# Performance work log

Measured on AMD Instinct MI355X. Metric: run time of the kernel, lower is better.

## Reference

```python
import jax, jax.numpy as jnp
import numpy as np

EPS = 1e-8
NEG = -1e7  # min_val used by masked_max


def _div_safe(a, b):
    return a / jnp.maximum(b, EPS)


def _masked_max(v, m, axis):
    mb = jnp.broadcast_to(m, v.shape)
    val = jnp.where(mb > 0, v, NEG).max(axis=axis)
    return val * mb.max(axis=axis)


def _masked_mean(v, m, axis):
    mb = jnp.broadcast_to(m, v.shape)
    return _div_safe((v * mb).sum(axis=axis), mb.sum(axis=axis))


def _cos_pairwise(v1, v2):
    # v1: (b,p,h), v2: (b,q,h) -> (b,p,q)
    n1 = jnp.linalg.norm(v1, axis=2, keepdims=True)
    n2 = jnp.linalg.norm(v2, axis=2, keepdims=True)
    dot = jnp.einsum('bph,bqh->bpq', v1, v2)
    return _div_safe(dot, n1 * n2.transpose(0, 2, 1))


def _mpm(v1, v2, w):
    # v1,v2: (b,L,h); w: (np,h) -> ((b,L,1), (b,L,np))
    dot = (v1 * v2).sum(-1)
    n = jnp.linalg.norm(v1, axis=-1) * jnp.linalg.norm(v2, axis=-1)
    mv1 = _div_safe(dot, n)[..., None]
    wv1 = w[None, None] * v1[:, :, None, :]  # (b,L,np,h)
    wv2 = w[None, None] * v2[:, :, None, :]
    dotm = (wv1 * wv2).sum(-1)
    nm = jnp.linalg.norm(wv1, axis=-1) * jnp.linalg.norm(wv2, axis=-1)
    return mv1, _div_safe(dotm, nm)


def _mpm_pairwise(v1, v2, w):
    # v1: (b,L1,h), v2: (b,L2,h), w: (np,h) -> (b,L1,L2,np)
    wv1 = w[None, :, None, :] * v1[:, None, :, :]  # (b,np,L1,h)
    wv2 = w[None, :, None, :] * v2[:, None, :, :]  # (b,np,L2,h)
    n1 = jnp.linalg.norm(wv1, axis=3, keepdims=True)
    n2 = jnp.linalg.norm(wv2, axis=3, keepdims=True)
    dot = jnp.einsum('bnph,bnqh->bnpq', wv1, wv2)
    res = _div_safe(dot, n1 * n2.transpose(0, 1, 3, 2))
    return res.transpose(0, 2, 3, 1)


def _bimpm(context_p, mask_p, context_h, mask_h, w_full, w_maxpool, w_att, w_max_att):
    b = context_p.shape[0]
    mask_p_h = mask_p[:, :, None] * mask_h[:, None, :]  # (b,Lp,Lh)
    mask_h_p = mask_p_h.transpose(0, 2, 1)
    context_p = context_p * mask_p[:, :, None]
    context_h = context_h * mask_h[:, :, None]

    cos = _cos_pairwise(context_p, context_h)  # (b,Lp,Lh)
    mv_p = [_masked_max(cos, mask_p_h, 2)[:, :, None],
            _masked_mean(cos, mask_p_h, 2)[:, :, None]]
    cos_t = cos.transpose(0, 2, 1)
    mv_h = [_masked_max(cos_t, mask_h_p, 2)[:, :, None],
            _masked_mean(cos_t, mask_h_p, 2)[:, :, None]]

    # full match (is_forward=True): match against last non-pad token
    idx_p = jnp.clip(mask_p.sum(1).astype(jnp.int32) - 1, 0)
    idx_h = jnp.clip(mask_h.sum(1).astype(jnp.int32) - 1, 0)
    last_p = context_p[jnp.arange(b), idx_p][:, None, :]  # (b,1,h)
    last_h = context_h[jnp.arange(b), idx_h][:, None, :]
    m1, mm = _mpm(context_p, jnp.broadcast_to(last_h, context_p.shape), w_full)
    mv_p += [m1, mm]
    m1, mm = _mpm(context_h, jnp.broadcast_to(last_p, context_h.shape), w_full)
    mv_h += [m1, mm]

    # maxpool match
    mv_max = _mpm_pairwise(context_p, context_h, w_maxpool)  # (b,Lp,Lh,np)
    mv_p += [_masked_max(mv_max, mask_p_h[..., None], 2),
             _masked_mean(mv_max, mask_p_h[..., None], 2)]
    mv_max_t = mv_max.transpose(0, 2, 1, 3)
    mv_h += [_masked_max(mv_max_t, mask_h_p[..., None], 2),
             _masked_mean(mv_max_t, mask_h_p[..., None], 2)]

    # attentive match
    att_h = context_h[:, None, :, :] * cos[..., None]  # (b,Lp,Lh,h)
    att_p = context_p[:, :, None, :] * cos[..., None]  # (b,Lp,Lh,h)
    att_mean_h = _div_safe(jnp.einsum('bpq,bqh->bph', cos, context_h),
                           cos.sum(2, keepdims=True))
    att_mean_p = _div_safe(jnp.einsum('bpq,bph->bqh', cos, context_p),
                           cos.sum(1, keepdims=True).transpose(0, 2, 1))
    m1, mm = _mpm(context_p, att_mean_h, w_att)
    mv_p += [m1, mm]
    m1, mm = _mpm(context_h, att_mean_p, w_att)
    mv_h += [m1, mm]

    # max attentive match
    att_max_h = _masked_max(att_h, mask_p_h[..., None], 2)  # (b,Lp,h)
    att_max_p = _masked_max(att_p.transpose(0, 2, 1, 3), mask_h_p[..., None], 2)  # (b,Lh,h)
    m1, mm = _mpm(context_p, att_max_h, w_max_att)
    mv_p += [m1, mm]
    m1, mm = _mpm(context_h, att_max_p, w_max_att)
    mv_h += [m1, mm]

    return jnp.concatenate(mv_p, axis=2), jnp.concatenate(mv_h, axis=2)


def setup_inputs() -> dict:
    B, LP, LH, H, NP = 32, 128, 128, 200, 20
    key = jax.random.key(0)
    ks = jax.random.split(key, 8)
    len_p = jax.random.randint(ks[0], (B,), LP // 2, LP + 1)
    len_h = jax.random.randint(ks[1], (B,), LH // 2, LH + 1)
    return {
        'context_p': jax.random.normal(ks[2], (B, LP, H), dtype=jnp.float32),
        'mask_p': (jnp.arange(LP)[None, :] < len_p[:, None]).astype(jnp.float32),
        'context_h': jax.random.normal(ks[3], (B, LH, H), dtype=jnp.float32),
        'mask_h': (jnp.arange(LH)[None, :] < len_h[:, None]).astype(jnp.float32),
        'w_full': jax.random.uniform(ks[4], (NP, H), dtype=jnp.float32),
        'w_maxpool': jax.random.uniform(ks[5], (NP, H), dtype=jnp.float32),
        'w_att': jax.random.uniform(ks[6], (NP, H), dtype=jnp.float32),
        'w_max_att': jax.random.uniform(ks[7], (NP, H), dtype=jnp.float32),
    }


def reference(context_p, mask_p, context_h, mask_h, w_full, w_maxpool, w_att, w_max_att):
    return _bimpm(context_p, mask_p, context_h, mask_h, w_full, w_maxpool, w_att, w_max_att)
```

## Files before the change

kernel.cpp:

```cpp
#include <hip/hip_runtime.h>
#include <hip/hip_bf16.h>


#define EPSF 1e-8f
#define NEGF -1e7f

constexpr int Bc = 32, Lc = 128, Hc = 200, NPc = 20, NCHc = 105;
constexpr int KP = 224;
constexpr size_t SLL = (size_t)Bc * Lc * Lc;

constexpr size_t OFF_COS    = 0;
constexpr size_t OFF_COST   = OFF_COS + SLL;
constexpr size_t OFF_NORMP  = OFF_COST + SLL;
constexpr size_t OFF_NORMH  = OFF_NORMP + (size_t)Bc * Lc;
constexpr size_t OFF_LENP   = OFF_NORMH + (size_t)Bc * Lc;
constexpr size_t OFF_LENH   = OFF_LENP + Bc;
constexpr size_t OFF_LASTP  = OFF_LENH + Bc;
constexpr size_t OFF_LASTH  = OFF_LASTP + (size_t)Bc * Hc;
constexpr size_t OFF_NWP    = OFF_LASTH + (size_t)Bc * Hc;
constexpr size_t OFF_NWH    = OFF_NWP + (size_t)Bc * NPc * Lc;
constexpr size_t OFF_MASKPF = OFF_NWH + (size_t)Bc * NPc * Lc;
constexpr size_t OFF_MASKHF = OFF_MASKPF + (size_t)Bc * Lc;
constexpr size_t OFF_FLAG   = OFF_MASKHF + (size_t)Bc * Lc;
constexpr size_t OFF_WT     = OFF_FLAG + 64;
constexpr size_t OFF_RPMAX  = OFF_WT + (size_t)Hc * 64;
constexpr size_t OFF_RPSUM  = OFF_RPMAX + 2 * (size_t)Bc * NPc * Lc;
constexpr size_t OFF_CPMAX  = OFF_RPSUM + 2 * (size_t)Bc * NPc * Lc;
constexpr size_t OFF_CPSUM  = OFF_CPMAX + 2 * (size_t)Bc * NPc * Lc;
constexpr size_t OFF_CHB    = OFF_CPSUM + 2 * (size_t)Bc * NPc * Lc;
constexpr size_t OFF_CPB    = OFF_CHB + ((size_t)Bc * Lc * KP) / 2;
constexpr size_t OFF_W2K    = OFF_CPB + ((size_t)Bc * Lc * KP) / 2;
constexpr size_t WS_FLOATS  = OFF_W2K + (size_t)NPc * KP;

typedef __attribute__((ext_vector_type(8))) short short8v;
typedef __attribute__((ext_vector_type(4))) float float4v;
typedef __attribute__((ext_vector_type(2))) float float2v;

__device__ __forceinline__ float loadf(const void* p, size_t i, int isb) {
  if (isb) return __bfloat162float(((const __hip_bfloat16*)p)[i]);
  return ((const float*)p)[i];
}

__device__ __forceinline__ void storef(void* out, size_t i, float v, int isb) {
  if (isb) ((__hip_bfloat16*)out)[i] = __float2bfloat16(v);
  else ((float*)out)[i] = v;
}

__device__ __forceinline__ float s2f(unsigned short s) {
  union { unsigned u; float f; } c;
  c.u = ((unsigned)s) << 16;
  return c.f;
}

__device__ __forceinline__ short b2s(float f) {
  __hip_bfloat16 h = __float2bfloat16(f);
  union { __hip_bfloat16 b; short s; } u;
  u.b = h;
  return u.s;
}

__device__ __forceinline__ short8v weight8(short8v a, float4v w0, float4v w1) {
  short8v r;
#pragma unroll
  for (int e = 0; e < 8; e++) {
    float w = (e < 4) ? w0[e] : w1[e - 4];
    r[e] = b2s(s2f((unsigned short)a[e]) * w);
  }
  return r;
}

__global__ __launch_bounds__(256) void prep_kernel(
    const void* __restrict__ cp_, const void* __restrict__ mp,
    const void* __restrict__ ch_, const void* __restrict__ mh,
    const void* __restrict__ wf, const void* __restrict__ wmp,
    const void* __restrict__ watt, const void* __restrict__ wma,
    float* __restrict__ ws) {
  int isb = (((const unsigned short*)mp)[0] == 0x3F80u) ? 1 : 0;
  int bid = blockIdx.x;
  int t = threadIdx.x;
  const int n0 = Bc * Lc;
  if (bid < 2048) {
    int g = bid * 4 + (t >> 6);
    int side = g >> 12;
    int bl = g & 4095;
    int b = bl >> 7, l = bl & 127;
    int lane = t & 63;
    const void* ctx = side ? ch_ : cp_;
    const void* maskin = side ? mh : mp;
    float mk = loadf(maskin, b * Lc + l, isb);
    size_t rowbase = ((size_t)b * Lc + l) * Hc;
    __hip_bfloat16* cb16 = (__hip_bfloat16*)(ws + (side ? OFF_CHB : OFF_CPB));
    size_t cb = ((size_t)b * Lc + l) * KP;

    float v[4];
    float ss = 0.f;
    for (int i = 0; i < 4; i++) {
      int h = lane + 64 * i;
      float x = 0.f;
      if (h < Hc) {
        x = loadf(ctx, rowbase + h, isb) * mk;
        cb16[cb + h] = __float2bfloat16(x);
      } else if (h < KP) {
        cb16[cb + h] = __float2bfloat16(0.f);
      }
      v[i] = x;
      ss += x * x;
    }
    for (int o = 32; o > 0; o >>= 1) ss += __shfl_xor(ss, o);
    if (lane == 0) ws[(side ? OFF_NORMH : OFF_NORMP) + b * Lc + l] = sqrtf(ss);

    float* nw = ws + (side ? OFF_NWH : OFF_NWP) + (size_t)b * NPc * Lc;
    for (int np_ = 0; np_ < NPc; np_++) {
      float s = 0.f;
      for (int i = 0; i < 4; i++) {
        int h = lane + 64 * i;
        if (h < Hc) {
          float w = loadf(wmp, (size_t)np_ * Hc + h, isb);
          float wx = w * v[i];
          s += wx * wx;
        }
      }
      for (int o = 32; o > 0; o >>= 1) s += __shfl_xor(s, o);
      if (lane == 0) nw[np_ * Lc + l] = sqrtf(s);
    }
    return;
  }
  int cb = bid - 2048;
  if (cb >= 100) {
    int idx = (cb - 100) * 4 + (t >> 6);
    int side = idx >> 5, b = idx & 31;
    int lane = t & 63;
    const void* mask = side ? mh : mp;
    const void* ctx = side ? ch_ : cp_;
    float s = 0.f;
    for (int l = lane; l < Lc; l += 64) s += loadf(mask, b * Lc + l, isb);
    for (int o = 32; o > 0; o >>= 1) s += __shfl_xor(s, o);
    if (lane == 0) ws[(side ? OFF_LENH : OFF_LENP) + b] = s;
    int lidx = (int)(s + 0.5f) - 1;
    if (lidx < 0) lidx = 0;
    float mk = loadf(mask, b * Lc + lidx, isb);
    float* lastv = ws + (side ? OFF_LASTH : OFF_LASTP) + (size_t)b * Hc;
    for (int h = lane; h < Hc; h += 64)
      lastv[h] = loadf(ctx, ((size_t)b * Lc + lidx) * Hc + h, isb) * mk;
    return;
  }
  int g = cb * 256 + t;
  if (g == 0) ws[OFF_FLAG] = (float)isb;
  if (g < n0) {
    ws[OFF_MASKPF + g] = loadf(mp, g, isb);
  } else if (g < 2 * n0) {
    ws[OFF_MASKHF + (g - n0)] = loadf(mh, g - n0, isb);
  } else if (g < 2 * n0 + 64 * Hc) {
    int r = g - 2 * n0;
    int h = r >> 6, c = r & 63;
    float w = 1.0f;
    if (c < 20) w = loadf(wf, (size_t)c * Hc + h, isb);
    else if (c < 40) w = loadf(watt, (size_t)(c - 20) * Hc + h, isb);
    else if (c < 60) w = loadf(wma, (size_t)(c - 40) * Hc + h, isb);
    ws[OFF_WT + r] = w * w;
  } else if (g < 2 * n0 + 64 * Hc + NPc * KP) {
    int r = g - (2 * n0 + 64 * Hc);
    int np_ = r / KP, k = r % KP;
    float w = (k < Hc) ? loadf(wmp, (size_t)np_ * Hc + k, isb) : 0.f;
    ws[OFF_W2K + r] = w * w;
  }
}

__global__ __launch_bounds__(64, 3) void maxpool_kernel(float* __restrict__ ws) {
  int b = blockIdx.x;
  int s = blockIdx.y;
  int np_ = blockIdx.z;
  int pi = s >> 1, qi = s & 1;
  int cosmode = (np_ == NPc);
  int lane = threadIdx.x;
  int rsel = lane & 15, quad = lane >> 4;

  const short* Ab = (const short*)(ws + OFF_CPB)
                  + ((size_t)b * Lc + pi * 64 + rsel) * KP + quad * 8;
  const short* Bb = (const short*)(ws + OFF_CHB)
                  + ((size_t)b * Lc + qi * 64 + rsel) * KP + quad * 8;
  const float* w2k = ws + OFF_W2K + (size_t)(cosmode ? 0 : np_) * KP + quad * 8;

  float4v acc[4][4];
  float4v zf = {0.f, 0.f, 0.f, 0.f};
#pragma unroll
  for (int i = 0; i < 4; i++)
#pragma unroll
    for (int j = 0; j < 4; j++) acc[i][j] = zf;

#pragma unroll
  for (int st = 0; st < 7; st++) {
    int k0 = st * 32;
    short8v bf4[4], af[4];
#pragma unroll
    for (int t = 0; t < 4; t++)
      bf4[t] = *(const short8v*)(Bb + (size_t)t * 16 * KP + k0);
    if (cosmode) {
#pragma unroll
      for (int t = 0; t < 4; t++)
        af[t] = *(const short8v*)(Ab + (size_t)t * 16 * KP + k0);
    } else {
      float4v w0 = *(const float4v*)(w2k + k0);
      float4v w1 = *(const float4v*)(w2k + k0 + 4);
#pragma unroll
      for (int t = 0; t < 4; t++) {
        short8v ar = *(const short8v*)(Ab + (size_t)t * 16 * KP + k0);
        af[t] = weight8(ar, w0, w1);
      }
    }
#pragma unroll
    for (int i = 0; i < 4; i++)
#pragma unroll
      for (int j = 0; j < 4; j++)
        acc[i][j] = __builtin_amdgcn_mfma_f32_16x16x32_bf16(af[i], bf4[j], acc[i][j], 0, 0, 0);
  }

  if (cosmode) {
    const float* npn = ws + OFF_NORMP + b * Lc + pi * 64;
    const float* nhn = ws + OFF_NORMH + b * Lc + qi * 64;
    float nh4[4];
#pragma unroll
    for (int tj = 0; tj < 4; tj++) nh4[tj] = nhn[tj * 16 + rsel];
    float* cosp = ws + OFF_COS + (size_t)b * Lc * Lc;
    float* cost = ws + OFF_COST + (size_t)b * Lc * Lc;
#pragma unroll
    for (int ti = 0; ti < 4; ti++) {
#pragma unroll
      for (int r = 0; r < 4; r++) {
        int prow = pi * 64 + ti * 16 + quad * 4 + r;
        float npv = npn[ti * 16 + quad * 4 + r];
#pragma unroll
        for (int tj = 0; tj < 4; tj++) {
          int qcol = qi * 64 + tj * 16 + rsel;
          float v = acc[ti][tj][r] * __builtin_amdgcn_rcpf(fmaxf(npv * nh4[tj], EPSF));
          cosp[(size_t)prow * Lc + qcol] = v;
          cost[(size_t)qcol * Lc + prow] = v;
        }
      }
    }
    return;
  }

  const float* nwp = ws + OFF_NWP + ((size_t)b * NPc + np_) * Lc + pi * 64;
  const float* nwh = ws + OFF_NWH + ((size_t)b * NPc + np_) * Lc + qi * 64;
  const float* maskP = ws + OFF_MASKPF + b * Lc + pi * 64;
  const float* maskH = ws + OFF_MASKHF + b * Lc + qi * 64;
  float nhv[4], mhv[4], cmax[4], csum[4];
#pragma unroll
  for (int tj = 0; tj < 4; tj++) {
    int q = tj * 16 + rsel;
    nhv[tj] = nwh[q];
    mhv[tj] = maskH[q];
    cmax[tj] = NEGF;
    csum[tj] = 0.f;
  }
  size_t rbase = (((size_t)qi * Bc + b) * NPc + np_) * Lc + pi * 64;
  size_t cbase = (((size_t)pi * Bc + b) * NPc + np_) * Lc + qi * 64;
#pragma unroll
  for (int ti = 0; ti < 4; ti++) {
#pragma unroll
    for (int r = 0; r < 4; r++) {
      int p = ti * 16 + quad * 4 + r;
      float npv = nwp[p], mpv = maskP[p];
      float rm = NEGF, rs = 0.f;
#pragma unroll
      for (int tj = 0; tj < 4; tj++) {
        float v = acc[ti][tj][r] * __builtin_amdgcn_rcpf(fmaxf(npv * nhv[tj], EPSF));
        if (mhv[tj] > 0.f) rm = fmaxf(rm, v);
        rs += v * mhv[tj];
        if (mpv > 0.f) cmax[tj] = fmaxf(cmax[tj], v);
        csum[tj] += v * mpv;
      }
#pragma unroll
      for (int o = 1; o <= 8; o <<= 1) {
        rm = fmaxf(rm, __shfl_xor(rm, o));
        rs += __shfl_xor(rs, o);
      }
      if (rsel == 0) {
        ws[OFF_RPMAX + rbase + p] = rm;
        ws[OFF_RPSUM + rbase + p] = rs;
      }
    }
  }
#pragma unroll
  for (int tj = 0; tj < 4; tj++) {
#pragma unroll
    for (int o = 16; o <= 32; o <<= 1) {
      cmax[tj] = fmaxf(cmax[tj], __shfl_xor(cmax[tj], o));
      csum[tj] += __shfl_xor(csum[tj], o);
    }
  }
  if (quad == 0) {
#pragma unroll
    for (int tj = 0; tj < 4; tj++) {
      int q = tj * 16 + rsel;
      ws[OFF_CPMAX + cbase + q] = cmax[tj];
      ws[OFF_CPSUM + cbase + q] = csum[tj];
    }
  }
}

__global__ __launch_bounds__(256) void attmpm_kernel(float* __restrict__ ws,
                                                     void* __restrict__ out) {
  int b = blockIdx.x;
  int r0 = blockIdx.y * 4;
  int side = blockIdx.z;
  int t = threadIdx.x;
  int isb = ws[OFF_FLAG] > 0.5f;
  const float* cosrows = ws + (side ? OFF_COST : OFF_COS) + ((size_t)b * Lc + r0) * Lc;
  const unsigned short* vsb = (const unsigned short*)(ws + (side ? OFF_CPB : OFF_CHB))
                            + (size_t)b * Lc * KP;
  const unsigned short* v1b = (const unsigned short*)(ws + (side ? OFF_CHB : OFF_CPB))
                            + ((size_t)b * Lc + r0) * KP;
  const float* vlast = ws + (side ? OFF_LASTP : OFF_LASTH) + (size_t)b * Hc;
  const float* maskRow = ws + (side ? OFF_MASKHF : OFF_MASKPF) + b * Lc;
  float lenOther = ws[(side ? OFF_LENP : OFF_LENH) + b];
  int lenO = (int)(lenOther + 0.5f);
  size_t obase = (size_t)side * Bc * Lc * NCHc + ((size_t)b * Lc + r0) * NCHc;

  __shared__ float crowT[Lc][4];
  __shared__ float dens[4];
  __shared__ float v1s[4][Hc];
  __shared__ float v2l[Hc];
  __shared__ float am[4][Hc];
  __shared__ float ax[4][Hc];
  for (int i = t; i < 4 * Lc; i += 256) {
    int row = i >> 7, q = i & 127;
    crowT[q][row] = cosrows[(size_t)row * Lc + q];
  }
  for (int i = t; i < 4 * Hc; i += 256) {
    int row = i / Hc, h = i % Hc;
    v1s[row][h] = s2f(v1b[(size_t)row * KP + h]);
  }
  for (int h = t; h < Hc; h += 256) v2l[h] = vlast[h];
  __syncthreads();

  int wv = t >> 6, lane = t & 63;
  {
    float x1 = crowT[lane][wv], x2 = crowT[lane + 64][wv];
    float sv = x1 + x2;
    float mv = fmaxf(x1, (lane + 64 < lenO) ? x2 : NEGF);
    for (int o = 32; o > 0; o >>= 1) {
      sv += __shfl_xor(sv, o);
      mv = fmaxf(mv, __shfl_xor(mv, o));
    }
    if (lane == 0) {
      dens[wv] = sv;
      float mr = maskRow[r0 + wv];
      storef(out, obase + (size_t)wv * NCHc + 0, mr * mv, isb);
      storef(out, obase + (size_t)wv * NCHc + 1, mr * sv / fmaxf(mr * lenOther, EPSF), isb);
    }
  }
  __syncthreads();

  if (t < Hc) {
    float2v s01 = {0.f, 0.f}, s23 = {0.f, 0.f};
    float2v m01 = {NEGF, NEGF}, m23 = {NEGF, NEGF};
    const unsigned short* vb = vsb + t;
    int q = 0;
    for (; q + 8 <= lenO; q += 8) {
      unsigned short raw[8];
#pragma unroll
      for (int j = 0; j < 8; j++) raw[j] = vb[(size_t)(q + j) * KP];
      float4 cc[8];
#pragma unroll
      for (int j = 0; j < 8; j++) cc[j] = *(const float4*)&crowT[q + j][0];
#pragma unroll
      for (int j = 0; j < 8; j++) {
        float pr = s2f(raw[j]);
        float2v pp = {pr, pr};
        float2v c01 = {cc[j].x, cc[j].y}, c23 = {cc[j].z, cc[j].w};
        float2v v01 = c01 * pp, v23 = c23 * pp;
        s01 += v01;
        s23 += v23;
        m01[0] = fmaxf(m01[0], v01[0]); m01[1] = fmaxf(m01[1], v01[1]);
        m23[0] = fmaxf(m23[0], v23[0]); m23[1] = fmaxf(m23[1], v23[1]);
      }
    }
    for (; q < lenO; q++) {
      float pr = s2f(vb[(size_t)q * KP]);
      float4 c4 = *(const float4*)&crowT[q][0];
      float2v pp = {pr, pr};
      float2v c01 = {c4.x, c4.y}, c23 = {c4.z, c4.w};
      float2v v01 = c01 * pp, v23 = c23 * pp;
      s01 += v01;
      s23 += v23;
      m01[0] = fmaxf(m01[0], v01[0]); m01[1] = fmaxf(m01[1], v01[1]);
      m23[0] = fmaxf(m23[0], v23[0]); m23[1] = fmaxf(m23[1], v23[1]);
    }
    am[0][t] = s01[0] / fmaxf(dens[0], EPSF);
    am[1][t] = s01[1] / fmaxf(dens[1], EPSF);
    am[2][t] = s23[0] / fmaxf(dens[2], EPSF);
    am[3][t] = s23[1] / fmaxf(dens[3], EPSF);
    ax[0][t] = maskRow[r0 + 0] * m01[0];
    ax[1][t] = maskRow[r0 + 1] * m01[1];
    ax[2][t] = maskRow[r0 + 2] * m23[0];
    ax[3][t] = maskRow[r0 + 3] * m23[1];
  }
  __syncthreads();

  int c = lane;
  int row = r0 + wv;
  size_t orow = obase + (size_t)wv * NCHc;

  if (c < NPc) {
    size_t PMX = side ? OFF_CPMAX : OFF_RPMAX;
    size_t PSM = side ? OFF_CPSUM : OFF_RPSUM;
    size_t i0 = (((size_t)0 * Bc + b) * NPc + c) * Lc + row;
    size_t i1 = (((size_t)1 * Bc + b) * NPc + c) * Lc + row;
    float m = fmaxf(ws[PMX + i0], ws[PMX + i1]);
    float sum = ws[PSM + i0] + ws[PSM + i1];
    float mk = maskRow[row];
    storef(out, orow + 23 + c, mk * m, isb);
    storef(out, orow + 43 + c, mk * sum / fmaxf(mk * lenOther, EPSF), isb);
  }

  int v2i = (c < 20) ? 0 : (c < 40) ? 1 : (c < 60) ? 2 : (c - 60);
  if (v2i > 2) v2i = 2;
  const float* y = (v2i == 0) ? v2l : (v2i == 1) ? am[wv] : ax[wv];
  const float* x = v1s[wv];
  const float* wtc = ws + OFF_WT + c;
  float2v sd = {0.f, 0.f}, sa = {0.f, 0.f}, sb = {0.f, 0.f};
#pragma unroll 2
  for (int h4 = 0; h4 < Hc / 4; h4++) {
    float w0 = wtc[(size_t)(h4 * 4 + 0) * 64];
    float w1 = wtc[(size_t)(h4 * 4 + 1) * 64];
    float w2 = wtc[(size_t)(h4 * 4 + 2) * 64];
    float w3 = wtc[(size_t)(h4 * 4 + 3) * 64];
    float4 xv = *(const float4*)&x[h4 * 4];
    float4 yv = *(const float4*)&y[h4 * 4];
    float2v wq0 = {w0, w1}, wq1 = {w2, w3};
    float2v x0 = {xv.x, xv.y}, x1 = {xv.z, xv.w};
    float2v y0 = {yv.x, yv.y}, y1 = {yv.z, yv.w};
    float2v t0 = wq0 * x0;
    sd += t0 * y0; sa += t0 * x0; sb += wq0 * (y0 * y0);
    t0 = wq1 * x1;
    sd += t0 * y1; sa += t0 * x1; sb += wq1 * (y1 * y1);
  }
  float sdf = sd[0] + sd[1], saf = sa[0] + sa[1], sbf = sb[0] + sb[1];
  float mm = sdf / fmaxf(sqrtf(saf) * sqrtf(sbf), EPSF);
  int ch;
  if (c < 20) ch = 3 + c;
  else if (c < 40) ch = 64 + (c - 20);
  else if (c < 60) ch = 85 + (c - 40);
  else if (c == 60) ch = 2;
  else if (c == 61) ch = 63;
  else if (c == 62) ch = 84;
  else ch = -1;
  if (ch >= 0) storef(out, orow + ch, mm, isb);
}

extern "C" void kernel_launch(void* const* d_in, const int* in_sizes, int n_in,
                              void* d_out, int out_size, void* d_ws, size_t ws_size,
                              hipStream_t stream) {
  const void* ctx_p = d_in[0];
  const void* mask_p = d_in[1];
  const void* ctx_h = d_in[2];
  const void* mask_h = d_in[3];
  const void* w_full = d_in[4];
  const void* w_mp = d_in[5];
  const void* w_att = d_in[6];
  const void* w_maxatt = d_in[7];
  float* ws = (float*)d_ws;

  prep_kernel<<<2164, 256, 0, stream>>>(ctx_p, mask_p, ctx_h, mask_h,
                                        w_full, w_mp, w_att, w_maxatt, ws);
  maxpool_kernel<<<dim3(Bc, 4, NPc + 1), 64, 0, stream>>>(ws);
  attmpm_kernel<<<dim3(Bc, Lc / 4, 2), 256, 0, stream>>>(ws, d_out);
}
```

Baseline: 153.1 us.

## Add transposed bf16 context layout and vectorize weight and row loads

The prep kernel gains extra blocks that write masked, transposed (h-major) bf16 copies of both contexts through a shared-memory tile. The attentive-mean loop can then read 8 consecutive sequence elements with one 16-byte load instead of strided scalar loads. The squared-weight table is re-laid out so that four consecutive h values for a channel sit together and load as a float4. The v1 row staging also uses 8-wide loads. The cost is more prep work, extra workspace, and a larger prep grid.

```diff
diff --git a/kernel.cpp b/kernel.cpp
--- a/kernel.cpp
+++ b/kernel.cpp
@@ -30,7 +30,9 @@
 constexpr size_t OFF_CHB    = OFF_CPSUM + 2 * (size_t)Bc * NPc * Lc;
 constexpr size_t OFF_CPB    = OFF_CHB + ((size_t)Bc * Lc * KP) / 2;
 constexpr size_t OFF_W2K    = OFF_CPB + ((size_t)Bc * Lc * KP) / 2;
-constexpr size_t WS_FLOATS  = OFF_W2K + (size_t)NPc * KP;
+constexpr size_t OFF_CTTP   = OFF_W2K + (size_t)NPc * KP;
+constexpr size_t OFF_CTTH   = OFF_CTTP + ((size_t)Bc * Hc * Lc) / 2;
+constexpr size_t WS_FLOATS  = OFF_CTTH + ((size_t)Bc * Hc * Lc) / 2;
 
 typedef __attribute__((ext_vector_type(8))) short short8v;
 typedef __attribute__((ext_vector_type(4))) float float4v;
@@ -75,6 +77,7 @@
     const void* __restrict__ wf, const void* __restrict__ wmp,
     const void* __restrict__ watt, const void* __restrict__ wma,
     float* __restrict__ ws) {
+  __shared__ float tile_s[32][33];
   int isb = (((const unsigned short*)mp)[0] == 0x3F80u) ? 1 : 0;
   int bid = blockIdx.x;
   int t = threadIdx.x;
@@ -126,6 +129,32 @@
     return;
   }
   int cb = bid - 2048;
+  if (cb >= 116) {
+    int tb = cb - 116;
+    int sb = tb / 28, tile = tb % 28;
+    int side = sb >> 5, b = sb & 31;
+    int h0 = (tile >> 2) * 32, l0 = (tile & 3) * 32;
+    const void* ctx = side ? ch_ : cp_;
+    const void* maskin = side ? mh : mp;
+    int tx = t & 31, ty = t >> 5;
+    for (int j = 0; j < 4; j++) {
+      int l = l0 + ty + j * 8, h = h0 + tx;
+      float x = 0.f;
+      if (h < Hc)
+        x = loadf(ctx, ((size_t)b * Lc + l) * Hc + h, isb)
+          * loadf(maskin, b * Lc + l, isb);
+      tile_s[ty + j * 8][tx] = x;
+    }
+    __syncthreads();
+    __hip_bfloat16* ctt = (__hip_bfloat16*)(ws + (side ? OFF_CTTH : OFF_CTTP));
+    for (int j = 0; j < 4; j++) {
+      int h = h0 + ty + j * 8, l = l0 + tx;
+      if (h < Hc)
+        ctt[(size_t)b * Hc * Lc + (size_t)h * Lc + l] =
+            __float2bfloat16(tile_s[tx][ty + j * 8]);
+    }
+    return;
+  }
   if (cb >= 100) {
     int idx = (cb - 100) * 4 + (t >> 6);
     int side = idx >> 5, b = idx & 31;
@@ -152,7 +181,8 @@
     ws[OFF_MASKHF + (g - n0)] = loadf(mh, g - n0, isb);
   } else if (g < 2 * n0 + 64 * Hc) {
     int r = g - 2 * n0;
-    int h = r >> 6, c = r & 63;
+    int h4 = r >> 8, c = (r >> 2) & 63, e = r & 3;
+    int h = h4 * 4 + e;
     float w = 1.0f;
     if (c < 20) w = loadf(wf, (size_t)c * Hc + h, isb);
     else if (c < 40) w = loadf(watt, (size_t)(c - 20) * Hc + h, isb);
@@ -308,8 +338,6 @@
   int t = threadIdx.x;
   int isb = ws[OFF_FLAG] > 0.5f;
   const float* cosrows = ws + (side ? OFF_COST : OFF_COS) + ((size_t)b * Lc + r0) * Lc;
-  const unsigned short* vsb = (const unsigned short*)(ws + (side ? OFF_CPB : OFF_CHB))
-                            + (size_t)b * Lc * KP;
   const unsigned short* v1b = (const unsigned short*)(ws + (side ? OFF_CHB : OFF_CPB))
                             + ((size_t)b * Lc + r0) * KP;
   const float* vlast = ws + (side ? OFF_LASTP : OFF_LASTH) + (size_t)b * Hc;
@@ -328,9 +356,11 @@
     int row = i >> 7, q = i & 127;
     crowT[q][row] = cosrows[(size_t)row * Lc + q];
   }
-  for (int i = t; i < 4 * Hc; i += 256) {
-    int row = i / Hc, h = i % Hc;
-    v1s[row][h] = s2f(v1b[(size_t)row * KP + h]);
+  if (t < 100) {
+    int row = t / 25, g8 = t % 25;
+    short8v rv = *(const short8v*)(v1b + (size_t)row * KP + g8 * 8);
+#pragma unroll
+    for (int e = 0; e < 8; e++) v1s[row][g8 * 8 + e] = s2f((unsigned short)rv[e]);
   }
   for (int h = t; h < Hc; h += 256) v2l[h] = vlast[h];
   __syncthreads();
@@ -356,18 +386,17 @@
   if (t < Hc) {
     float2v s01 = {0.f, 0.f}, s23 = {0.f, 0.f};
     float2v m01 = {NEGF, NEGF}, m23 = {NEGF, NEGF};
-    const unsigned short* vb = vsb + t;
+    const unsigned short* vbt = (const unsigned short*)(ws + (side ? OFF_CTTP : OFF_CTTH))
+                              + (size_t)b * Hc * Lc + (size_t)t * Lc;
     int q = 0;
     for (; q + 8 <= lenO; q += 8) {
-      unsigned short raw[8];
-#pragma unroll
-      for (int j = 0; j < 8; j++) raw[j] = vb[(size_t)(q + j) * KP];
+      short8v rv = *(const short8v*)(vbt + q);
       float4 cc[8];
 #pragma unroll
       for (int j = 0; j < 8; j++) cc[j] = *(const float4*)&crowT[q + j][0];
 #pragma unroll
       for (int j = 0; j < 8; j++) {
-        float pr = s2f(raw[j]);
+        float pr = s2f((unsigned short)rv[j]);
         float2v pp = {pr, pr};
         float2v c01 = {cc[j].x, cc[j].y}, c23 = {cc[j].z, cc[j].w};
         float2v v01 = c01 * pp, v23 = c23 * pp;
@@ -378,7 +407,7 @@
       }
     }
     for (; q < lenO; q++) {
-      float pr = s2f(vb[(size_t)q * KP]);
+      float pr = s2f(vbt[q]);
       float4 c4 = *(const float4*)&crowT[q][0];
       float2v pp = {pr, pr};
       float2v c01 = {c4.x, c4.y}, c23 = {c4.z, c4.w};
@@ -419,17 +448,14 @@
   if (v2i > 2) v2i = 2;
   const float* y = (v2i == 0) ? v2l : (v2i == 1) ? am[wv] : ax[wv];
   const float* x = v1s[wv];
-  const float* wtc = ws + OFF_WT + c;
+  const float* wt4 = ws + OFF_WT;
   float2v sd = {0.f, 0.f}, sa = {0.f, 0.f}, sb = {0.f, 0.f};
 #pragma unroll 2
   for (int h4 = 0; h4 < Hc / 4; h4++) {
-    float w0 = wtc[(size_t)(h4 * 4 + 0) * 64];
-    float w1 = wtc[(size_t)(h4 * 4 + 1) * 64];
-    float w2 = wtc[(size_t)(h4 * 4 + 2) * 64];
-    float w3 = wtc[(size_t)(h4 * 4 + 3) * 64];
+    float4 wq = *(const float4*)&wt4[((size_t)h4 * 64 + c) * 4];
     float4 xv = *(const float4*)&x[h4 * 4];
     float4 yv = *(const float4*)&y[h4 * 4];
-    float2v wq0 = {w0, w1}, wq1 = {w2, w3};
+    float2v wq0 = {wq.x, wq.y}, wq1 = {wq.z, wq.w};
     float2v x0 = {xv.x, xv.y}, x1 = {xv.z, xv.w};
     float2v y0 = {yv.x, yv.y}, y1 = {yv.z, yv.w};
     float2v t0 = wq0 * x0;
@@ -463,7 +489,7 @@
   const void* w_maxatt = d_in[7];
   float* ws = (float*)d_ws;
 
-  prep_kernel<<<2164, 256, 0, stream>>>(ctx_p, mask_p, ctx_h, mask_h,
+  prep_kernel<<<3956, 256, 0, stream>>>(ctx_p, mask_p, ctx_h, mask_h,
                                         w_full, w_mp, w_att, w_maxatt, ws);
   maxpool_kernel<<<dim3(Bc, 4, NPc + 1), 64, 0, stream>>>(ws);
   attmpm_kernel<<<dim3(Bc, Lc / 4, 2), 256, 0, stream>>>(ws, d_out);
```

New measurement: 161.2 us. +5.3%, slower.
